# Kernel optimization log

Measured on AMD Instinct MI355X. Metric: run time of the kernel, lower is better.

The kernel has to match this reference:

```python
import jax, jax.numpy as jnp
import numpy as np

HIDDEN = 4096
N_HEADS = 32
N_KV_HEADS = 8
HEAD_SIZE = HIDDEN // N_HEADS  # 128
ROPE_THETA = 10000.0
SEQ_LEN = 1024
BATCH = 4


def setup_inputs() -> dict:
    key = jax.random.key(0)
    k1, k2, k3 = jax.random.split(key, 3)
    scale = 1.0 / np.sqrt(HIDDEN)
    hidden_states = jax.random.normal(k1, (BATCH * SEQ_LEN, HIDDEN), dtype=jnp.float32)
    w_qkv = jax.random.normal(k2, ((N_HEADS + 2 * N_KV_HEADS) * HEAD_SIZE, HIDDEN), dtype=jnp.float32) * scale
    w_o = jax.random.normal(k3, (HIDDEN, N_HEADS * HEAD_SIZE), dtype=jnp.float32) * scale
    return {"hidden_states": hidden_states, "w_qkv": w_qkv, "w_o": w_o, "seq_len": SEQ_LEN}


def _rope(x, pos, theta):
    # x: [B, S, H, D]; pos: [S] absolute positions; rotate-half (LLAMA/NeoX) style
    d = x.shape[-1]
    inv_freq = 1.0 / (theta ** (jnp.arange(0, d, 2, dtype=jnp.float32) / d))  # [D/2]
    ang = pos.astype(jnp.float32)[:, None] * inv_freq[None, :]  # [S, D/2]
    cos = jnp.cos(ang)[None, :, None, :]
    sin = jnp.sin(ang)[None, :, None, :]
    x1, x2 = jnp.split(x, 2, axis=-1)
    return jnp.concatenate([x1 * cos - x2 * sin, x2 * cos + x1 * sin], axis=-1)


def reference(hidden_states, w_qkv, w_o, seq_len):
    total, hidden = hidden_states.shape
    B = total // seq_len
    hd = HEAD_SIZE
    # fused QKV projection (bias-free), split like the torch module
    qkv = hidden_states @ w_qkv.T  # [T, (H+2K)*hd]
    q, k, v = jnp.split(qkv, [N_HEADS * hd, (N_HEADS + N_KV_HEADS) * hd], axis=1)
    q = q.reshape(B, seq_len, N_HEADS, hd)
    k = k.reshape(B, seq_len, N_KV_HEADS, hd)
    v = v.reshape(B, seq_len, N_KV_HEADS, hd)
    # inline RoPE (ROPE_LLAMA) on q and k at absolute positions
    pos = jnp.arange(seq_len)
    q = _rope(q, pos, ROPE_THETA)
    k = _rope(k, pos, ROPE_THETA)
    # GQA: map each q head to its kv head (kv_head_mapping = repeat_interleave)
    groups = N_HEADS // N_KV_HEADS
    k = jnp.repeat(k, groups, axis=2)  # [B, S, H, hd]
    v = jnp.repeat(v, groups, axis=2)
    scale = hd ** -0.5
    scores = jnp.einsum('bqhd,bkhd->bhqk', q, k) * scale  # [B, H, S, S]
    causal = jnp.tril(jnp.ones((seq_len, seq_len), dtype=bool))
    scores = jnp.where(causal[None, None], scores, jnp.finfo(scores.dtype).min)
    probs = jax.nn.softmax(scores, axis=-1)
    attn = jnp.einsum('bhqk,bkhd->bqhd', probs, v).reshape(total, N_HEADS * hd)
    return attn @ w_o.T  # [T, hidden]
```

## Files before the change

### kernel.cpp

```cpp
#include <hip/hip_runtime.h>


typedef short bf16x8 __attribute__((ext_vector_type(8)));
typedef short bf16x4 __attribute__((ext_vector_type(4)));
typedef float floatx4 __attribute__((ext_vector_type(4)));
typedef float floatx16 __attribute__((ext_vector_type(16)));
typedef unsigned short u16x4 __attribute__((ext_vector_type(4)));

__device__ __forceinline__ unsigned short f2bf(float f) {
  unsigned u = __float_as_uint(f);
  u += 0x7FFFu + ((u >> 16) & 1u);
  return (unsigned short)(u >> 16);
}
__device__ __forceinline__ float bf2f(unsigned short h) {
  return __uint_as_float(((unsigned)h) << 16);
}

__device__ __forceinline__ void async16(const void* g, void* l) {
  __builtin_amdgcn_global_load_lds(
      (const __attribute__((address_space(1))) unsigned int*)g,
      (__attribute__((address_space(3))) unsigned int*)l, 16, 0, 0);
}

__global__ void cvt_f32_bf16(const float4* __restrict__ in,
                             u16x4* __restrict__ out, int n4) {
  int i = blockIdx.x * 256 + threadIdx.x;
  if (i < n4) {
    float4 v = in[i];
    u16x4 o;
    o.x = f2bf(v.x); o.y = f2bf(v.y); o.z = f2bf(v.z); o.w = f2bf(v.w);
    out[i] = o;
  }
}

template <int OUT_BF16>
__global__ __launch_bounds__(256) void gemm_bt32(
    const unsigned short* __restrict__ A, const unsigned short* __restrict__ B,
    void* __restrict__ Cout, int M, int N, int K) {
  __shared__ __align__(16) unsigned short As[128 * 64];
  __shared__ __align__(16) unsigned short Bs[128 * 64];
  const int tid = threadIdx.x;
  const int wave = tid >> 6, lane = tid & 63;
  const int l32 = lane & 31, hi = lane >> 5;
  const int bm = blockIdx.y << 7, bn = blockIdx.x << 7;
  const int wm = (wave >> 1) << 6, wn = (wave & 1) << 6;

  floatx16 acc[2][2];
#pragma unroll
  for (int mi = 0; mi < 2; ++mi)
#pragma unroll
    for (int ni = 0; ni < 2; ++ni)
#pragma unroll
      for (int r = 0; r < 16; ++r) acc[mi][ni][r] = 0.f;

  const int srow = lane >> 3;
  const int schunk = (lane & 7) ^ srow;
  const unsigned short* Asrc[4];
  const unsigned short* Bsrc[4];
  char* lA[4];
  char* lB[4];
#pragma unroll
  for (int j = 0; j < 4; ++j) {
    int blk = wave + 4 * j;
    Asrc[j] = A + (size_t)(bm + blk * 8 + srow) * K + schunk * 8;
    Bsrc[j] = B + (size_t)(bn + blk * 8 + srow) * K + schunk * 8;
    lA[j] = (char*)As + wave * 1024 + j * 4096;
    lB[j] = (char*)Bs + wave * 1024 + j * 4096;
  }

  const unsigned short* Ap = As + (wm + l32) * 64;
  const unsigned short* Bp = Bs + (wn + l32) * 64;
  int co[4];
#pragma unroll
  for (int k = 0; k < 4; ++k) co[k] = ((k * 2 + hi) ^ (lane & 7)) * 8;

  for (int k0 = 0; k0 < K; k0 += 64) {
    __syncthreads();
#pragma unroll
    for (int j = 0; j < 4; ++j) async16(Asrc[j] + k0, lA[j]);
#pragma unroll
    for (int j = 0; j < 4; ++j) async16(Bsrc[j] + k0, lB[j]);
    __syncthreads();
    bf16x8 af[2][4], bfr[2][4];
#pragma unroll
    for (int mi = 0; mi < 2; ++mi)
#pragma unroll
      for (int k = 0; k < 4; ++k)
        af[mi][k] = *(const bf16x8*)(Ap + mi * 2048 + co[k]);
#pragma unroll
    for (int ni = 0; ni < 2; ++ni)
#pragma unroll
      for (int k = 0; k < 4; ++k)
        bfr[ni][k] = *(const bf16x8*)(Bp + ni * 2048 + co[k]);
#pragma unroll
    for (int k = 0; k < 4; ++k)
#pragma unroll
      for (int mi = 0; mi < 2; ++mi)
#pragma unroll
        for (int ni = 0; ni < 2; ++ni)
          acc[mi][ni] = __builtin_amdgcn_mfma_f32_32x32x16_bf16(
              af[mi][k], bfr[ni][k], acc[mi][ni], 0, 0, 0);
  }

  const int col0 = bn + wn + l32;
#pragma unroll
  for (int mi = 0; mi < 2; ++mi)
#pragma unroll
    for (int ni = 0; ni < 2; ++ni)
#pragma unroll
      for (int reg = 0; reg < 16; ++reg) {
        int row = bm + wm + mi * 32 + 4 * hi + (reg & 3) + 8 * (reg >> 2);
        if (OUT_BF16)
          ((unsigned short*)Cout)[(size_t)row * N + col0 + ni * 32] =
              f2bf(acc[mi][ni][reg]);
        else
          ((float*)Cout)[(size_t)row * N + col0 + ni * 32] = acc[mi][ni][reg];
      }
}

__global__ void rope_k_kernel(unsigned short* __restrict__ qkv) {
  const int t = blockIdx.x;
  const int s = t & 1023;
  const int head = 32 + blockIdx.y * 4 + (threadIdx.x >> 6);
  const int d = threadIdx.x & 63;
  unsigned short* p = qkv + (size_t)t * 6144 + head * 128;
  float x1 = bf2f(p[d]), x2 = bf2f(p[d + 64]);
  float inv_freq = exp2f((float)d * -0.20762050593046015f);
  float ang = (float)s * inv_freq;
  float c, sn;
  __sincosf(ang, &sn, &c);
  p[d] = f2bf(x1 * c - x2 * sn);
  p[d + 64] = f2bf(x2 * c + x1 * sn);
}

__global__ __launch_bounds__(256, 3) void flash_attn(
    const unsigned short* __restrict__ qkv, unsigned short* __restrict__ aout) {
  const int pr = blockIdx.x;
  const int h = blockIdx.y, b = blockIdx.z;
  const int kh = h >> 2;
  const int tid = threadIdx.x;
  const int wave = tid >> 6, lane = tid & 63;
  const int quad = lane >> 4, l16 = lane & 15;

  __shared__ __align__(16) unsigned short Ks[64][136];
  __shared__ __align__(16) unsigned short Vt[128][68];
  __shared__ __align__(16) unsigned short Ps[64][68];

  const int krow = tid >> 4, kcol = (tid & 15) << 3;
  const int vrb = (tid & 15) << 2, vcol = (tid >> 4) << 3;
  const unsigned short* kp = qkv + (size_t)(b << 10) * 6144 + 4096 + kh * 128;
  const unsigned short* vp = qkv + (size_t)(b << 10) * 6144 + 5120 + kh * 128;

  for (int half = 0; half < 2; ++half) {
    const int qt = half ? pr : 15 - pr;
    const int q0 = qt << 6;

    bf16x8 qf[4];
    {
      const int qrow = q0 + wave * 16 + l16;
      const unsigned short* qp =
          qkv + (size_t)((b << 10) + qrow) * 6144 + h * 128 + quad * 8;
#pragma unroll
      for (int ks = 0; ks < 4; ++ks) qf[ks] = *(const bf16x8*)(qp + ks * 32);
      const float pos = (float)qrow;
      const float scale = 0.08838834764831845f;
#pragma unroll
      for (int ks = 0; ks < 2; ++ks)
#pragma unroll
        for (int e = 0; e < 8; ++e) {
          int d = ks * 32 + quad * 8 + e;
          float ang = pos * exp2f((float)d * -0.20762050593046015f);
          float c, sn;
          __sincosf(ang, &sn, &c);
          float x1 = bf2f((unsigned short)qf[ks][e]);
          float x2 = bf2f((unsigned short)qf[ks + 2][e]);
          qf[ks][e] = (short)f2bf((x1 * c - x2 * sn) * scale);
          qf[ks + 2][e] = (short)f2bf((x2 * c + x1 * sn) * scale);
        }
    }

    floatx4 o_acc[8];
#pragma unroll
    for (int i = 0; i < 8; ++i) o_acc[i] = (floatx4){0.f, 0.f, 0.f, 0.f};
    float l_lane[4] = {0.f, 0.f, 0.f, 0.f};

    bf16x8 kreg[4], vreg[4];
#pragma unroll
    for (int j = 0; j < 4; ++j)
      kreg[j] = *(const bf16x8*)(kp + (size_t)(krow + j * 16) * 6144 + kcol);
#pragma unroll
    for (int j = 0; j < 4; ++j)
      vreg[j] = *(const bf16x8*)(vp + (size_t)(vrb + j) * 6144 + vcol);

    for (int t = 0; t <= qt; ++t) {
      __syncthreads();
#pragma unroll
      for (int j = 0; j < 4; ++j)
        *(bf16x8*)&Ks[krow + j * 16][kcol] = kreg[j];
#pragma unroll
      for (int e = 0; e < 8; ++e) {
        bf16x4 w = {vreg[0][e], vreg[1][e], vreg[2][e], vreg[3][e]};
        *(bf16x4*)&Vt[vcol + e][vrb] = w;
      }
      __syncthreads();
      if (t < qt) {
        const size_t nb = (size_t)((t + 1) << 6) * 6144;
#pragma unroll
        for (int j = 0; j < 4; ++j)
          kreg[j] =
              *(const bf16x8*)(kp + nb + (size_t)(krow + j * 16) * 6144 + kcol);
#pragma unroll
        for (int j = 0; j < 4; ++j)
          vreg[j] = *(const bf16x8*)(vp + nb + (size_t)(vrb + j) * 6144 + vcol);
      }

      floatx4 sacc[4];
#pragma unroll
      for (int ni = 0; ni < 4; ++ni) sacc[ni] = (floatx4){0.f, 0.f, 0.f, 0.f};
#pragma unroll
      for (int ks = 0; ks < 4; ++ks)
#pragma unroll
        for (int ni = 0; ni < 4; ++ni) {
          bf16x8 kf = *(const bf16x8*)&Ks[ni * 16 + l16][ks * 32 + quad * 8];
          sacc[ni] = __builtin_amdgcn_mfma_f32_16x16x32_bf16(qf[ks], kf,
                                                             sacc[ni], 0, 0, 0);
        }

      const bool masked = (t == qt);
#pragma unroll
      for (int r = 0; r < 4; ++r) {
        float rs = 0.f;
#pragma unroll
        for (int ni = 0; ni < 4; ++ni) {
          float e = __expf(sacc[ni][r]);
          if (masked && (ni * 16 + l16) > (wave * 16 + quad * 4 + r)) e = 0.f;
          rs += e;
          Ps[wave * 16 + quad * 4 + r][ni * 16 + l16] = f2bf(e);
        }
        l_lane[r] += rs;
      }
      asm volatile("s_waitcnt lgkmcnt(0)" ::: "memory");

#pragma unroll
      for (int ks2 = 0; ks2 < 2; ++ks2) {
        bf16x8 pf = *(const bf16x8*)&Ps[wave * 16 + l16][ks2 * 32 + quad * 8];
#pragma unroll
        for (int n8 = 0; n8 < 8; ++n8) {
          bf16x8 vf = *(const bf16x8*)&Vt[n8 * 16 + l16][ks2 * 32 + quad * 8];
          o_acc[n8] = __builtin_amdgcn_mfma_f32_16x16x32_bf16(pf, vf, o_acc[n8],
                                                              0, 0, 0);
        }
      }
    }

#pragma unroll
    for (int r = 0; r < 4; ++r) {
      float l = l_lane[r];
#pragma unroll
      for (int off = 1; off < 16; off <<= 1) l += __shfl_xor(l, off, 64);
      float inv = 1.0f / l;
      int row = q0 + wave * 16 + quad * 4 + r;
      unsigned short* op = aout + (size_t)((b << 10) + row) * 4096 + h * 128;
#pragma unroll
      for (int n8 = 0; n8 < 8; ++n8)
        op[n8 * 16 + l16] = f2bf(o_acc[n8][r] * inv);
    }
  }
}

extern "C" void kernel_launch(void* const* d_in, const int* in_sizes, int n_in,
                              void* d_out, int out_size, void* d_ws,
                              size_t ws_size, hipStream_t stream) {
  const float* X = (const float*)d_in[0];
  const float* Wqkv = (const float*)d_in[1];
  const float* Wo = (const float*)d_in[2];
  (void)in_sizes; (void)n_in; (void)out_size; (void)ws_size;

  char* ws = (char*)d_ws;
  unsigned short* Wqkvb = (unsigned short*)ws;
  unsigned short* AttnB = (unsigned short*)ws;
  unsigned short* Xb = (unsigned short*)(ws + 50331648);
  unsigned short* Wob = (unsigned short*)(ws + 50331648);
  unsigned short* QKVb = (unsigned short*)(ws + 83886080);

  cvt_f32_bf16<<<16384, 256, 0, stream>>>((const float4*)X, (u16x4*)Xb, 4194304);
  cvt_f32_bf16<<<24576, 256, 0, stream>>>((const float4*)Wqkv, (u16x4*)Wqkvb, 6291456);
  gemm_bt32<1><<<dim3(48, 32), 256, 0, stream>>>(Xb, Wqkvb, QKVb, 4096, 6144, 4096);
  rope_k_kernel<<<dim3(4096, 2), 256, 0, stream>>>(QKVb);
  cvt_f32_bf16<<<16384, 256, 0, stream>>>((const float4*)Wo, (u16x4*)Wob, 4194304);
  flash_attn<<<dim3(8, 32, 4), 256, 0, stream>>>(QKVb, AttnB);
  gemm_bt32<0><<<dim3(32, 32), 256, 0, stream>>>(AttnB, Wob, d_out, 4096, 4096, 4096);
}
```

Measured before the change: 699.2 us.

## Replace GEMM with 256x256 tile, multi-stage async LDS pipeline kernel

Replaces the 128x128, 4-wave GEMM with a 256x256-tile, 8-wave kernel using 16x16x32 bf16 MFMAs. It keeps a 4-slot LDS ring buffer with K-slices of 32 and prefetches two slices ahead through async global-to-LDS loads. Loads are interleaved with MFMA phases, using barriers and s_setprio to keep the matrix units busy. The larger tile raises arithmetic intensity and hides memory latency. In exchange it needs a large LDS footprint, and the QKV GEMM grid (384 blocks) covers the CUs unevenly, which may leave some idle in the last wave.

New measurement: 694.2 us. About the same (-0.7%).

```diff
diff --git a/kernel.cpp b/kernel.cpp
--- a/kernel.cpp
+++ b/kernel.cpp
@@ -4,7 +4,6 @@
 typedef short bf16x8 __attribute__((ext_vector_type(8)));
 typedef short bf16x4 __attribute__((ext_vector_type(4)));
 typedef float floatx4 __attribute__((ext_vector_type(4)));
-typedef float floatx16 __attribute__((ext_vector_type(16)));
 typedef unsigned short u16x4 __attribute__((ext_vector_type(4)));
 
 __device__ __forceinline__ unsigned short f2bf(float f) {
@@ -34,88 +33,117 @@
 }
 
 template <int OUT_BF16>
-__global__ __launch_bounds__(256) void gemm_bt32(
+__global__ __launch_bounds__(512, 2) void gemm256(
     const unsigned short* __restrict__ A, const unsigned short* __restrict__ B,
     void* __restrict__ Cout, int M, int N, int K) {
-  __shared__ __align__(16) unsigned short As[128 * 64];
-  __shared__ __align__(16) unsigned short Bs[128 * 64];
+  __shared__ __align__(16) unsigned short As[4][8192];
+  __shared__ __align__(16) unsigned short Bs[4][8192];
   const int tid = threadIdx.x;
   const int wave = tid >> 6, lane = tid & 63;
-  const int l32 = lane & 31, hi = lane >> 5;
-  const int bm = blockIdx.y << 7, bn = blockIdx.x << 7;
-  const int wm = (wave >> 1) << 6, wn = (wave & 1) << 6;
-
-  floatx16 acc[2][2];
-#pragma unroll
-  for (int mi = 0; mi < 2; ++mi)
-#pragma unroll
-    for (int ni = 0; ni < 2; ++ni)
-#pragma unroll
-      for (int r = 0; r < 16; ++r) acc[mi][ni][r] = 0.f;
-
-  const int srow = lane >> 3;
-  const int schunk = (lane & 7) ^ srow;
-  const unsigned short* Asrc[4];
-  const unsigned short* Bsrc[4];
-  char* lA[4];
-  char* lB[4];
-#pragma unroll
-  for (int j = 0; j < 4; ++j) {
-    int blk = wave + 4 * j;
-    Asrc[j] = A + (size_t)(bm + blk * 8 + srow) * K + schunk * 8;
-    Bsrc[j] = B + (size_t)(bn + blk * 8 + srow) * K + schunk * 8;
-    lA[j] = (char*)As + wave * 1024 + j * 4096;
-    lB[j] = (char*)Bs + wave * 1024 + j * 4096;
-  }
-
-  const unsigned short* Ap = As + (wm + l32) * 64;
-  const unsigned short* Bp = Bs + (wn + l32) * 64;
-  int co[4];
-#pragma unroll
-  for (int k = 0; k < 4; ++k) co[k] = ((k * 2 + hi) ^ (lane & 7)) * 8;
-
-  for (int k0 = 0; k0 < K; k0 += 64) {
-    __syncthreads();
-#pragma unroll
-    for (int j = 0; j < 4; ++j) async16(Asrc[j] + k0, lA[j]);
-#pragma unroll
-    for (int j = 0; j < 4; ++j) async16(Bsrc[j] + k0, lB[j]);
-    __syncthreads();
-    bf16x8 af[2][4], bfr[2][4];
-#pragma unroll
-    for (int mi = 0; mi < 2; ++mi)
-#pragma unroll
-      for (int k = 0; k < 4; ++k)
-        af[mi][k] = *(const bf16x8*)(Ap + mi * 2048 + co[k]);
-#pragma unroll
-    for (int ni = 0; ni < 2; ++ni)
-#pragma unroll
-      for (int k = 0; k < 4; ++k)
-        bfr[ni][k] = *(const bf16x8*)(Bp + ni * 2048 + co[k]);
-#pragma unroll
-    for (int k = 0; k < 4; ++k)
-#pragma unroll
-      for (int mi = 0; mi < 2; ++mi)
-#pragma unroll
-        for (int ni = 0; ni < 2; ++ni)
-          acc[mi][ni] = __builtin_amdgcn_mfma_f32_32x32x16_bf16(
-              af[mi][k], bfr[ni][k], acc[mi][ni], 0, 0, 0);
-  }
-
-  const int col0 = bn + wn + l32;
-#pragma unroll
-  for (int mi = 0; mi < 2; ++mi)
-#pragma unroll
-    for (int ni = 0; ni < 2; ++ni)
-#pragma unroll
-      for (int reg = 0; reg < 16; ++reg) {
-        int row = bm + wm + mi * 32 + 4 * hi + (reg & 3) + 8 * (reg >> 2);
+  const int wm = wave >> 2, wn = wave & 3;
+  const int l16 = lane & 15, c4 = lane >> 4;
+  const int bm = blockIdx.y << 8, bn = blockIdx.x << 8;
+
+  int afOff[8], bfOff[4];
+#pragma unroll
+  for (int mi = 0; mi < 8; ++mi) {
+    int r = wm * 128 + mi * 16 + l16;
+    int pr = r >> 1, l8 = ((r & 1) << 2) | c4;
+    afOff[mi] = pr * 128 + ((l8 ^ (pr & 7)) << 4);
+  }
+#pragma unroll
+  for (int ni = 0; ni < 4; ++ni) {
+    int r = wn * 64 + ni * 16 + l16;
+    int pr = r >> 1, l8 = ((r & 1) << 2) | c4;
+    bfOff[ni] = pr * 128 + ((l8 ^ (pr & 7)) << 4);
+  }
+
+  const int sp = lane >> 3;
+  const int l8s = (lane & 7) ^ sp;
+  const int so = l8s >> 2, sc = (l8s & 3) << 3;
+  const unsigned short* aS0 = A + (size_t)(bm + wave * 16 + sp * 2 + so) * K + sc;
+  const unsigned short* aS1 = A + (size_t)(bm + (wave + 8) * 16 + sp * 2 + so) * K + sc;
+  const unsigned short* bS0 = B + (size_t)(bn + wave * 16 + sp * 2 + so) * K + sc;
+  const unsigned short* bS1 = B + (size_t)(bn + (wave + 8) * 16 + sp * 2 + so) * K + sc;
+  const int dst0 = wave * 1024, dst1 = (wave + 8) * 1024;
+
+  floatx4 acc[8][4];
+#pragma unroll
+  for (int mi = 0; mi < 8; ++mi)
+#pragma unroll
+    for (int ni = 0; ni < 4; ++ni) acc[mi][ni] = (floatx4){0.f, 0.f, 0.f, 0.f};
+
+  const int NT = K >> 5;
+  async16(aS0, (char*)As[0] + dst0);
+  async16(aS1, (char*)As[0] + dst1);
+  async16(bS0, (char*)Bs[0] + dst0);
+  async16(bS1, (char*)Bs[0] + dst1);
+  async16(aS0 + 32, (char*)As[1] + dst0);
+  async16(aS1 + 32, (char*)As[1] + dst1);
+  async16(bS0 + 32, (char*)Bs[1] + dst0);
+  async16(bS1 + 32, (char*)Bs[1] + dst1);
+  asm volatile("s_waitcnt vmcnt(4)" ::: "memory");
+  __builtin_amdgcn_s_barrier();
+
+  size_t koff = 64;
+  for (int t = 0; t < NT; ++t) {
+    const char* aB = (const char*)As[t & 3];
+    const char* bB = (const char*)Bs[t & 3];
+    char* aD = (char*)As[(t + 2) & 3];
+    char* bD = (char*)Bs[(t + 2) & 3];
+    const bool st = (t + 2) < NT;
+
+    bf16x8 af[8], bf[4];
+#pragma unroll
+    for (int mi = 0; mi < 4; ++mi) af[mi] = *(const bf16x8*)(aB + afOff[mi]);
+#pragma unroll
+    for (int ni = 0; ni < 4; ++ni) bf[ni] = *(const bf16x8*)(bB + bfOff[ni]);
+    if (st) { async16(aS0 + koff, aD + dst0); async16(aS1 + koff, aD + dst1); }
+    __builtin_amdgcn_s_barrier();
+    __builtin_amdgcn_s_setprio(1);
+#pragma unroll
+    for (int mi = 0; mi < 4; ++mi)
+#pragma unroll
+      for (int ni = 0; ni < 4; ++ni)
+        acc[mi][ni] = __builtin_amdgcn_mfma_f32_16x16x32_bf16(
+            af[mi], bf[ni], acc[mi][ni], 0, 0, 0);
+    __builtin_amdgcn_s_setprio(0);
+    __builtin_amdgcn_s_barrier();
+
+#pragma unroll
+    for (int mi = 4; mi < 8; ++mi) af[mi] = *(const bf16x8*)(aB + afOff[mi]);
+    if (st) { async16(bS0 + koff, bD + dst0); async16(bS1 + koff, bD + dst1); }
+    __builtin_amdgcn_s_barrier();
+    __builtin_amdgcn_s_setprio(1);
+#pragma unroll
+    for (int mi = 4; mi < 8; ++mi)
+#pragma unroll
+      for (int ni = 0; ni < 4; ++ni)
+        acc[mi][ni] = __builtin_amdgcn_mfma_f32_16x16x32_bf16(
+            af[mi], bf[ni], acc[mi][ni], 0, 0, 0);
+    __builtin_amdgcn_s_setprio(0);
+    if (st) asm volatile("s_waitcnt vmcnt(4)" ::: "memory");
+    else    asm volatile("s_waitcnt vmcnt(0)" ::: "memory");
+    __builtin_amdgcn_s_barrier();
+    koff += 32;
+  }
+
+  const int col0 = bn + wn * 64 + l16;
+#pragma unroll
+  for (int mi = 0; mi < 8; ++mi) {
+    const int row0 = bm + wm * 128 + mi * 16 + c4 * 4;
+#pragma unroll
+    for (int ni = 0; ni < 4; ++ni)
+#pragma unroll
+      for (int r = 0; r < 4; ++r) {
         if (OUT_BF16)
-          ((unsigned short*)Cout)[(size_t)row * N + col0 + ni * 32] =
-              f2bf(acc[mi][ni][reg]);
+          ((unsigned short*)Cout)[(size_t)(row0 + r) * N + col0 + ni * 16] =
+              f2bf(acc[mi][ni][r]);
         else
-          ((float*)Cout)[(size_t)row * N + col0 + ni * 32] = acc[mi][ni][reg];
-      }
+          ((float*)Cout)[(size_t)(row0 + r) * N + col0 + ni * 16] =
+              acc[mi][ni][r];
+      }
+  }
 }
 
 __global__ void rope_k_kernel(unsigned short* __restrict__ qkv) {
@@ -285,9 +313,9 @@
 
   cvt_f32_bf16<<<16384, 256, 0, stream>>>((const float4*)X, (u16x4*)Xb, 4194304);
   cvt_f32_bf16<<<24576, 256, 0, stream>>>((const float4*)Wqkv, (u16x4*)Wqkvb, 6291456);
-  gemm_bt32<1><<<dim3(48, 32), 256, 0, stream>>>(Xb, Wqkvb, QKVb, 4096, 6144, 4096);
+  gemm256<1><<<dim3(24, 16), 512, 0, stream>>>(Xb, Wqkvb, QKVb, 4096, 6144, 4096);
   rope_k_kernel<<<dim3(4096, 2), 256, 0, stream>>>(QKVb);
   cvt_f32_bf16<<<16384, 256, 0, stream>>>((const float4*)Wo, (u16x4*)Wob, 4194304);
   flash_attn<<<dim3(8, 32, 4), 256, 0, stream>>>(QKVb, AttnB);
-  gemm_bt32<0><<<dim3(32, 32), 256, 0, stream>>>(AttnB, Wob, d_out, 4096, 4096, 4096);
-}
+  gemm256<0><<<dim3(16, 16), 512, 0, stream>>>(AttnB, Wob, d_out, 4096, 4096, 4096);
+}
```
